# Optimization experiments

Measured on AMD Instinct MI355X. Metric: run time of the kernel, lower is better.

## Reference

```python
import jax, jax.numpy as jnp
import numpy as np

B, T, D = 2, 2048, 2048
H, KV = 16, 4
HD = D // H            # 128
REP = H // KV          # 4 query heads per kv head


def setup_inputs() -> dict:
    key = jax.random.key(0)
    ks = jax.random.split(key, 5)
    scale = D ** -0.5
    x = jax.random.normal(ks[0], (B, T, D), dtype=jnp.float32)
    Wq = jax.random.normal(ks[1], (D, H * HD), dtype=jnp.float32) * scale
    Wk = jax.random.normal(ks[2], (D, KV * HD), dtype=jnp.float32) * scale
    Wv = jax.random.normal(ks[3], (D, KV * HD), dtype=jnp.float32) * scale
    Wo = jax.random.normal(ks[4], (H * HD, D), dtype=jnp.float32) * scale
    return {"x": x, "Wq": Wq, "Wk": Wk, "Wv": Wv, "Wo": Wo}


def reference(x, Wq, Wk, Wv, Wo):
    b, t, d = x.shape
    # projections; group query heads by their kv head (repeat_interleave order:
    # q head h uses kv head h // REP, i.e. heads are contiguous per group)
    q = (x @ Wq).reshape(b, t, KV, REP, HD)          # bt(g r)d -> b t g r d
    k = (x @ Wk).reshape(b, t, KV, HD)
    v = (x @ Wv).reshape(b, t, KV, HD)
    # scores: [B, KV, REP, T, T] -- equivalent to repeat_interleave of kv heads
    scores = jnp.einsum('btgrd,bsgd->bgrts', q, k) * (HD ** -0.5)
    causal = jnp.tril(jnp.ones((t, t), dtype=bool))
    scores = jnp.where(causal, scores, -jnp.inf)
    weights = jax.nn.softmax(scores, axis=-1)
    out = jnp.einsum('bgrts,bsgd->btgrd', weights, v).reshape(b, t, H * HD)
    return jnp.round(out @ Wo, decimals=4)
```

## Files before the change

### kernel.cpp

```cpp
#include <hip/hip_runtime.h>
#include <hip/hip_bf16.h>
#include <math.h>

#define B_ 2
#define T_ 2048
#define D_ 2048
#define H_ 16
#define KV_ 4
#define HD_ 128
#define REP_ 4
#define QKVSTR 3072

typedef __attribute__((ext_vector_type(8))) short s16x8;
typedef __attribute__((ext_vector_type(4))) float f32x4;
typedef __hip_bfloat16 bf16;

__device__ __forceinline__ short f2bf(float x) {
    bf16 h = __float2bfloat16(x);
    return *reinterpret_cast<short*>(&h);
}

__device__ __forceinline__ void gl2lds16(const void* g, void* l) {
    __builtin_amdgcn_global_load_lds(
        (const __attribute__((address_space(1))) char*)g,
        (__attribute__((address_space(3))) char*)l, 16, 0, 0);
}

__global__ __launch_bounds__(256) void cast_bf16(const float* __restrict__ X,
                                                 bf16* __restrict__ Y, int n) {
    int i = (blockIdx.x * 256 + threadIdx.x) * 8;
    if (i >= n) return;
    float4 a = *(const float4*)(X + i);
    float4 b = *(const float4*)(X + i + 4);
    short o[8] = {f2bf(a.x), f2bf(a.y), f2bf(a.z), f2bf(a.w),
                  f2bf(b.x), f2bf(b.y), f2bf(b.z), f2bf(b.w)};
    *(s16x8*)(Y + i) = *(const s16x8*)o;
}

__global__ __launch_bounds__(256) void transpose_cast(const float* __restrict__ W,
                                                      bf16* __restrict__ Wt,
                                                      int K, int N, float scale) {
    __shared__ short tile[64 * 72];
    const int k0 = blockIdx.x * 64, n0 = blockIdx.y * 64;
    const int t = threadIdx.x;
    const int r = t >> 2, c0 = (t & 3) * 16;
    const float* src = W + (size_t)(k0 + r) * N + n0 + c0;
    #pragma unroll
    for (int i = 0; i < 16; i += 4) {
        float4 v = *(const float4*)(src + i);
        tile[r * 72 + c0 + i + 0] = f2bf(v.x * scale);
        tile[r * 72 + c0 + i + 1] = f2bf(v.y * scale);
        tile[r * 72 + c0 + i + 2] = f2bf(v.z * scale);
        tile[r * 72 + c0 + i + 3] = f2bf(v.w * scale);
    }
    __syncthreads();
    short tmp[16];
    #pragma unroll
    for (int i = 0; i < 16; ++i) tmp[i] = tile[(c0 + i) * 72 + r];
    bf16* dst = Wt + (size_t)(n0 + r) * K + k0 + c0;
    *(s16x8*)(dst)     = *(const s16x8*)&tmp[0];
    *(s16x8*)(dst + 8) = *(const s16x8*)&tmp[8];
}

__global__ __launch_bounds__(256) void transpose_v(const bf16* __restrict__ V,
                                                   bf16* __restrict__ Vtg) {
    __shared__ short tile[64 * 72];
    const int t0 = blockIdx.x * 64;
    const int g = blockIdx.y >> 1;
    const int dp = (blockIdx.y & 1) * 64;
    const int b = blockIdx.z;
    const int t = threadIdx.x;
    const int r = t >> 2, c0 = (t & 3) * 16;
    const bf16* src = V + (size_t)(b * T_ + t0 + r) * QKVSTR + g * HD_ + dp + c0;
    *(s16x8*)&tile[r * 72 + c0]     = *(const s16x8*)(src);
    *(s16x8*)&tile[r * 72 + c0 + 8] = *(const s16x8*)(src + 8);
    __syncthreads();
    const int d = t >> 2, tc = (t & 3) * 16;
    short tmp[16];
    #pragma unroll
    for (int i = 0; i < 16; ++i) tmp[i] = tile[(tc + i) * 72 + d];
    bf16* dst = Vtg + (size_t)((b * KV_ + g) * HD_ + dp + d) * T_ + t0 + tc;
    *(s16x8*)(dst)     = *(const s16x8*)&tmp[0];
    *(s16x8*)(dst + 8) = *(const s16x8*)&tmp[8];
}

template<typename OUTT, int ROUND>
__global__ __launch_bounds__(256) void gemm_nt(const bf16* __restrict__ A,
                                               const bf16* __restrict__ Bt,
                                               OUTT* __restrict__ C,
                                               int M, int N, int K) {
    __shared__ short As[128 * 64];
    __shared__ short Bs[128 * 64];
    const int tid = threadIdx.x;
    const int lane = tid & 63;
    const int wave = tid >> 6;
    const int quad = lane >> 4;
    const int l16 = lane & 15;
    const int wr = wave >> 1, wc = wave & 1;
    const int row0 = blockIdx.y * 128;
    const int col0 = blockIdx.x * 128;

    f32x4 acc[4][4] = {};

    for (int k0 = 0; k0 < K; k0 += 64) {
        __syncthreads();
        #pragma unroll
        for (int i = 0; i < 4; ++i) {
            int g = i * 256 + tid;
            int row = g >> 3;
            int cs = (g & 7) ^ (row & 7);
            gl2lds16(A + (size_t)(row0 + row) * K + k0 + cs * 8, &As[g * 8]);
        }
        #pragma unroll
        for (int i = 0; i < 4; ++i) {
            int g = i * 256 + tid;
            int row = g >> 3;
            int cs = (g & 7) ^ (row & 7);
            gl2lds16(Bt + (size_t)(col0 + row) * K + k0 + cs * 8, &Bs[g * 8]);
        }
        __syncthreads();
        #pragma unroll
        for (int kk = 0; kk < 2; ++kk) {
            s16x8 af[4], bfr[4];
            #pragma unroll
            for (int i = 0; i < 4; ++i) {
                int row = wr * 64 + i * 16 + l16;
                int c = (kk * 4 + quad) ^ (row & 7);
                af[i] = *(const s16x8*)&As[row * 64 + c * 8];
            }
            #pragma unroll
            for (int j = 0; j < 4; ++j) {
                int row = wc * 64 + j * 16 + l16;
                int c = (kk * 4 + quad) ^ (row & 7);
                bfr[j] = *(const s16x8*)&Bs[row * 64 + c * 8];
            }
            #pragma unroll
            for (int i = 0; i < 4; ++i)
                #pragma unroll
                for (int j = 0; j < 4; ++j)
                    acc[i][j] = __builtin_amdgcn_mfma_f32_16x16x32_bf16(
                        af[i], bfr[j], acc[i][j], 0, 0, 0);
        }
    }

    #pragma unroll
    for (int i = 0; i < 4; ++i) {
        #pragma unroll
        for (int j = 0; j < 4; ++j) {
            #pragma unroll
            for (int r = 0; r < 4; ++r) {
                int row = row0 + wr * 64 + i * 16 + quad * 4 + r;
                int col = col0 + wc * 64 + j * 16 + l16;
                float v = acc[i][j][r];
                if (ROUND) v = rintf(v * 1e4f) * 1e-4f;
                if constexpr (sizeof(OUTT) == 2)
                    C[(size_t)row * N + col] = __float2bfloat16(v);
                else
                    C[(size_t)row * N + col] = v;
            }
        }
    }
}

__global__ __launch_bounds__(256, 3) void flash3(const bf16* __restrict__ Q,
                                                 const bf16* __restrict__ K,
                                                 const bf16* __restrict__ Vtg,
                                                 bf16* __restrict__ O) {
    __shared__ short Kt[64 * 128];
    __shared__ short Vt[128 * 64];
    __shared__ short PsOb[64 * 136];
    __shared__ float lbuf[4][16];

    const int h = blockIdx.x;
    const int b = blockIdx.y & 1;
    const int qt = 31 - (blockIdx.y >> 1);
    const int g = h >> 2;
    const int tid = threadIdx.x;
    const int lane = tid & 63;
    const int wave = tid >> 6;
    const int quad = lane >> 4;
    const int l16 = lane & 15;
    const int q0g = qt * 64 + wave * 16;

    s16x8 qf[4];
    {
        const bf16* qp = Q + (size_t)(b * T_ + q0g + l16) * QKVSTR + h * HD_ + quad * 8;
        #pragma unroll
        for (int ks = 0; ks < 4; ++ks) qf[ks] = *(const s16x8*)(qp + ks * 32);
    }

    const bf16* Kp = K + (size_t)(b * T_) * QKVSTR + g * HD_;
    const bf16* Vp = Vtg + (size_t)((b * KV_ + g) * HD_) * T_;

    float l_part[4] = {0.f, 0.f, 0.f, 0.f};
    f32x4 oacc[8] = {};

    for (int j = 0; j <= qt; ++j) {
        const int s0 = j * 64;
        __syncthreads();
        #pragma unroll
        for (int i = 0; i < 4; ++i) {
            int g2 = i * 256 + tid;
            int s = g2 >> 4;
            int cs = (g2 & 15) ^ (s & 15);
            gl2lds16(Kp + (size_t)(s0 + s) * QKVSTR + cs * 8, &Kt[g2 * 8]);
        }
        #pragma unroll
        for (int i = 0; i < 4; ++i) {
            int g2 = i * 256 + tid;
            int d = g2 >> 3;
            int cs = (g2 & 7) ^ (d & 7);
            gl2lds16(Vp + (size_t)d * T_ + s0 + cs * 8, &Vt[g2 * 8]);
        }
        __syncthreads();

        f32x4 sacc[4] = {};
        #pragma unroll
        for (int ks = 0; ks < 4; ++ks) {
            s16x8 kf[4];
            #pragma unroll
            for (int ct = 0; ct < 4; ++ct) {
                int srow = ct * 16 + l16;
                int c = (ks * 4 + quad) ^ (srow & 15);
                kf[ct] = *(const s16x8*)&Kt[srow * 128 + c * 8];
            }
            #pragma unroll
            for (int ct = 0; ct < 4; ++ct)
                sacc[ct] = __builtin_amdgcn_mfma_f32_16x16x32_bf16(
                    qf[ks], kf[ct], sacc[ct], 0, 0, 0);
        }

        const bool diag = (j == qt);
        #pragma unroll
        for (int r = 0; r < 4; ++r) {
            const int qrow = q0g + quad * 4 + r;
            if (diag) {
                #pragma unroll
                for (int ct = 0; ct < 4; ++ct)
                    if (s0 + ct * 16 + l16 > qrow) sacc[ct][r] = -INFINITY;
            }
            float psum = 0.f;
            #pragma unroll
            for (int ct = 0; ct < 4; ++ct) {
                float p = exp2f(sacc[ct][r]);
                sacc[ct][r] = p;
                psum += p;
            }
            l_part[r] += psum;
        }

        #pragma unroll
        for (int ct = 0; ct < 4; ++ct)
            #pragma unroll
            for (int r = 0; r < 4; ++r)
                PsOb[(wave * 16 + quad * 4 + r) * 72 + ct * 16 + l16] = f2bf(sacc[ct][r]);

        #pragma unroll
        for (int kk = 0; kk < 2; ++kk) {
            const s16x8 pf = *(const s16x8*)&PsOb[(wave * 16 + l16) * 72 + kk * 32 + quad * 8];
            #pragma unroll
            for (int dt = 0; dt < 8; ++dt) {
                int d = dt * 16 + l16;
                int c = (kk * 4 + quad) ^ (d & 7);
                const s16x8 vf = *(const s16x8*)&Vt[d * 64 + c * 8];
                oacc[dt] = __builtin_amdgcn_mfma_f32_16x16x32_bf16(
                    vf, pf, oacc[dt], 0, 0, 0);
            }
        }
    }

    #pragma unroll
    for (int r = 0; r < 4; ++r) {
        float v = l_part[r];
        v += __shfl_xor(v, 1);
        v += __shfl_xor(v, 2);
        v += __shfl_xor(v, 4);
        v += __shfl_xor(v, 8);
        l_part[r] = v;
    }
    if (l16 == 0) {
        #pragma unroll
        for (int r = 0; r < 4; ++r) lbuf[wave][quad * 4 + r] = l_part[r];
    }
    const float invl = 1.f / lbuf[wave][l16];

    __syncthreads();

    #pragma unroll
    for (int dt = 0; dt < 8; ++dt) {
        short tmp[4];
        #pragma unroll
        for (int r = 0; r < 4; ++r) tmp[r] = f2bf(oacc[dt][r] * invl);
        *(long long*)&PsOb[(wave * 16 + l16) * 136 + dt * 16 + quad * 4] =
            *(const long long*)tmp;
    }
    const int r2 = wave * 16 + (lane >> 2);
    bf16* op = O + (size_t)(b * T_ + qt * 64 + r2) * (H_ * HD_) + h * HD_;
    #pragma unroll
    for (int c = 0; c < 4; ++c) {
        int chunk = c * 4 + (lane & 3);
        *(s16x8*)(op + chunk * 8) = *(const s16x8*)&PsOb[r2 * 136 + chunk * 8];
    }
}

extern "C" void kernel_launch(void* const* d_in, const int* in_sizes, int n_in,
                              void* d_out, int out_size, void* d_ws, size_t ws_size,
                              hipStream_t stream) {
    const float* x  = (const float*)d_in[0];
    const float* Wq = (const float*)d_in[1];
    const float* Wk = (const float*)d_in[2];
    const float* Wv = (const float*)d_in[3];
    const float* Wo = (const float*)d_in[4];
    float* out = (float*)d_out;

    const size_t NR = (size_t)B_ * T_;
    bf16* ws = (bf16*)d_ws;
    bf16* xb    = ws;
    bf16* Wqkvt = xb + NR * D_;
    bf16* Wot   = Wqkvt + (size_t)QKVSTR * D_;
    bf16* QKVb  = Wot + (size_t)D_ * D_;
    bf16* Vtg   = QKVb + NR * QKVSTR;
    bf16* Ab    = Vtg + (size_t)B_ * KV_ * HD_ * T_;

    const float qscale = 1.4426950408889634f / sqrtf((float)HD_);

    cast_bf16<<<4096, 256, 0, stream>>>(x, xb, (int)(NR * D_));
    transpose_cast<<<dim3(32, 32), 256, 0, stream>>>(Wq, Wqkvt, D_, H_ * HD_, qscale);
    transpose_cast<<<dim3(32, 8),  256, 0, stream>>>(Wk, Wqkvt + (size_t)2048 * D_, D_, KV_ * HD_, 1.f);
    transpose_cast<<<dim3(32, 8),  256, 0, stream>>>(Wv, Wqkvt + (size_t)2560 * D_, D_, KV_ * HD_, 1.f);
    transpose_cast<<<dim3(32, 32), 256, 0, stream>>>(Wo, Wot, H_ * HD_, D_, 1.f);

    gemm_nt<bf16, 0><<<dim3(QKVSTR / 128, NR / 128), 256, 0, stream>>>(
        xb, Wqkvt, QKVb, (int)NR, QKVSTR, D_);

    transpose_v<<<dim3(T_ / 64, 8, B_), 256, 0, stream>>>(QKVb + 2560, Vtg);

    flash3<<<dim3(H_, 64, 1), 256, 0, stream>>>(QKVb, QKVb + 2048, Vtg, Ab);

    gemm_nt<float, 1><<<dim3(D_ / 128, NR / 128), 256, 0, stream>>>(
        Ab, Wot, out, (int)NR, D_, H_ * HD_);
}
```

Baseline: 290.7 us.

## Merge prep kernels, shrink flash LDS for higher occupancy, reorder query tiles

The five cast and transpose launches are merged into one prep kernel that dispatches on block index, which cuts launch overhead. The flash kernel now shares one LDS buffer between K, V, P and the output staging, packs P into a swizzled 64-wide layout instead of a padded one, and replaces the LDS row-sum exchange with lane shuffles. Together these lower LDS use so four blocks per CU fit instead of three. Query tiles are scheduled in a zigzag order to balance causal work, at the cost of different ordering across the grid.

```diff
diff --git a/kernel.cpp b/kernel.cpp
--- a/kernel.cpp
+++ b/kernel.cpp
@@ -26,23 +26,33 @@
         (__attribute__((address_space(3))) char*)l, 16, 0, 0);
 }
 
-__global__ __launch_bounds__(256) void cast_bf16(const float* __restrict__ X,
-                                                 bf16* __restrict__ Y, int n) {
-    int i = (blockIdx.x * 256 + threadIdx.x) * 8;
-    if (i >= n) return;
-    float4 a = *(const float4*)(X + i);
-    float4 b = *(const float4*)(X + i + 4);
-    short o[8] = {f2bf(a.x), f2bf(a.y), f2bf(a.z), f2bf(a.w),
-                  f2bf(b.x), f2bf(b.y), f2bf(b.z), f2bf(b.w)};
-    *(s16x8*)(Y + i) = *(const s16x8*)o;
-}
-
-__global__ __launch_bounds__(256) void transpose_cast(const float* __restrict__ W,
-                                                      bf16* __restrict__ Wt,
-                                                      int K, int N, float scale) {
+__global__ __launch_bounds__(256) void prep(const float* __restrict__ x,
+                                            const float* __restrict__ Wq,
+                                            const float* __restrict__ Wk,
+                                            const float* __restrict__ Wv,
+                                            const float* __restrict__ Wo,
+                                            bf16* __restrict__ xb,
+                                            bf16* __restrict__ Wqkvt,
+                                            bf16* __restrict__ Wot,
+                                            float qscale) {
+    const int bid = blockIdx.x;
+    const int t = threadIdx.x;
+    if (bid < 4096) {
+        int i = (bid * 256 + t) * 8;
+        float4 a = *(const float4*)(x + i);
+        float4 b = *(const float4*)(x + i + 4);
+        short o[8] = {f2bf(a.x), f2bf(a.y), f2bf(a.z), f2bf(a.w),
+                      f2bf(b.x), f2bf(b.y), f2bf(b.z), f2bf(b.w)};
+        *(s16x8*)(xb + i) = *(const s16x8*)o;
+        return;
+    }
     __shared__ short tile[64 * 72];
-    const int k0 = blockIdx.x * 64, n0 = blockIdx.y * 64;
-    const int t = threadIdx.x;
+    const float* W; bf16* dst; int N; float scale; int seg;
+    if (bid < 5120)      { seg = bid - 4096; W = Wq; dst = Wqkvt;                      N = 2048; scale = qscale; }
+    else if (bid < 5376) { seg = bid - 5120; W = Wk; dst = Wqkvt + (size_t)2048 * D_;  N = 512;  scale = 1.f; }
+    else if (bid < 5632) { seg = bid - 5376; W = Wv; dst = Wqkvt + (size_t)2560 * D_;  N = 512;  scale = 1.f; }
+    else                 { seg = bid - 5632; W = Wo; dst = Wot;                        N = 2048; scale = 1.f; }
+    const int k0 = (seg & 31) * 64, n0 = (seg >> 5) * 64;
     const int r = t >> 2, c0 = (t & 3) * 16;
     const float* src = W + (size_t)(k0 + r) * N + n0 + c0;
     #pragma unroll
@@ -57,9 +67,9 @@
     short tmp[16];
     #pragma unroll
     for (int i = 0; i < 16; ++i) tmp[i] = tile[(c0 + i) * 72 + r];
-    bf16* dst = Wt + (size_t)(n0 + r) * K + k0 + c0;
-    *(s16x8*)(dst)     = *(const s16x8*)&tmp[0];
-    *(s16x8*)(dst + 8) = *(const s16x8*)&tmp[8];
+    bf16* d = dst + (size_t)(n0 + r) * D_ + k0 + c0;
+    *(s16x8*)(d)     = *(const s16x8*)&tmp[0];
+    *(s16x8*)(d + 8) = *(const s16x8*)&tmp[8];
 }
 
 __global__ __launch_bounds__(256) void transpose_v(const bf16* __restrict__ V,
@@ -162,18 +172,18 @@
     }
 }
 
-__global__ __launch_bounds__(256, 3) void flash3(const bf16* __restrict__ Q,
+__global__ __launch_bounds__(256, 4) void flash6(const bf16* __restrict__ Q,
                                                  const bf16* __restrict__ K,
                                                  const bf16* __restrict__ Vtg,
                                                  bf16* __restrict__ O) {
-    __shared__ short Kt[64 * 128];
-    __shared__ short Vt[128 * 64];
-    __shared__ short PsOb[64 * 136];
-    __shared__ float lbuf[4][16];
+    __shared__ short smem[20480];
 
     const int h = blockIdx.x;
-    const int b = blockIdx.y & 1;
-    const int qt = 31 - (blockIdx.y >> 1);
+    const int by = blockIdx.y;
+    const int b = by & 1;
+    const int u = by >> 1;
+    const int s_ = u >> 3, v_ = u & 7;
+    const int qt = (s_ >> 1) * 16 + ((s_ & 1) ? (15 - v_) : v_);
     const int g = h >> 2;
     const int tid = threadIdx.x;
     const int lane = tid & 63;
@@ -203,14 +213,14 @@
             int g2 = i * 256 + tid;
             int s = g2 >> 4;
             int cs = (g2 & 15) ^ (s & 15);
-            gl2lds16(Kp + (size_t)(s0 + s) * QKVSTR + cs * 8, &Kt[g2 * 8]);
+            gl2lds16(Kp + (size_t)(s0 + s) * QKVSTR + cs * 8, &smem[g2 * 8]);
         }
         #pragma unroll
         for (int i = 0; i < 4; ++i) {
             int g2 = i * 256 + tid;
             int d = g2 >> 3;
             int cs = (g2 & 7) ^ (d & 7);
-            gl2lds16(Vp + (size_t)d * T_ + s0 + cs * 8, &Vt[g2 * 8]);
+            gl2lds16(Vp + (size_t)d * T_ + s0 + cs * 8, &smem[8192 + g2 * 8]);
         }
         __syncthreads();
 
@@ -222,7 +232,7 @@
             for (int ct = 0; ct < 4; ++ct) {
                 int srow = ct * 16 + l16;
                 int c = (ks * 4 + quad) ^ (srow & 15);
-                kf[ct] = *(const s16x8*)&Kt[srow * 128 + c * 8];
+                kf[ct] = *(const s16x8*)&smem[srow * 128 + c * 8];
             }
             #pragma unroll
             for (int ct = 0; ct < 4; ++ct)
@@ -252,17 +262,22 @@
         #pragma unroll
         for (int ct = 0; ct < 4; ++ct)
             #pragma unroll
-            for (int r = 0; r < 4; ++r)
-                PsOb[(wave * 16 + quad * 4 + r) * 72 + ct * 16 + l16] = f2bf(sacc[ct][r]);
+            for (int r = 0; r < 4; ++r) {
+                int row = wave * 16 + quad * 4 + r;
+                int chunk = (ct * 2 + (l16 >> 3)) ^ (row & 7);
+                smem[16384 + row * 64 + chunk * 8 + (l16 & 7)] = f2bf(sacc[ct][r]);
+            }
 
         #pragma unroll
         for (int kk = 0; kk < 2; ++kk) {
-            const s16x8 pf = *(const s16x8*)&PsOb[(wave * 16 + l16) * 72 + kk * 32 + quad * 8];
+            int prow = wave * 16 + l16;
+            int pc = (kk * 4 + quad) ^ (prow & 7);
+            const s16x8 pf = *(const s16x8*)&smem[16384 + prow * 64 + pc * 8];
             #pragma unroll
             for (int dt = 0; dt < 8; ++dt) {
                 int d = dt * 16 + l16;
                 int c = (kk * 4 + quad) ^ (d & 7);
-                const s16x8 vf = *(const s16x8*)&Vt[d * 64 + c * 8];
+                const s16x8 vf = *(const s16x8*)&smem[8192 + d * 64 + c * 8];
                 oacc[dt] = __builtin_amdgcn_mfma_f32_16x16x32_bf16(
                     vf, pf, oacc[dt], 0, 0, 0);
             }
@@ -271,18 +286,21 @@
 
     #pragma unroll
     for (int r = 0; r < 4; ++r) {
-        float v = l_part[r];
-        v += __shfl_xor(v, 1);
-        v += __shfl_xor(v, 2);
-        v += __shfl_xor(v, 4);
-        v += __shfl_xor(v, 8);
-        l_part[r] = v;
-    }
-    if (l16 == 0) {
-        #pragma unroll
-        for (int r = 0; r < 4; ++r) lbuf[wave][quad * 4 + r] = l_part[r];
-    }
-    const float invl = 1.f / lbuf[wave][l16];
+        float x = l_part[r];
+        x += __shfl_xor(x, 1);
+        x += __shfl_xor(x, 2);
+        x += __shfl_xor(x, 4);
+        x += __shfl_xor(x, 8);
+        l_part[r] = x;
+    }
+    const int srcl = (l16 >> 2) << 4;
+    const float lv0 = __shfl(l_part[0], srcl);
+    const float lv1 = __shfl(l_part[1], srcl);
+    const float lv2 = __shfl(l_part[2], srcl);
+    const float lv3 = __shfl(l_part[3], srcl);
+    const int rsel = l16 & 3;
+    const float lsel = rsel == 0 ? lv0 : rsel == 1 ? lv1 : rsel == 2 ? lv2 : lv3;
+    const float invl = 1.f / lsel;
 
     __syncthreads();
 
@@ -291,7 +309,7 @@
         short tmp[4];
         #pragma unroll
         for (int r = 0; r < 4; ++r) tmp[r] = f2bf(oacc[dt][r] * invl);
-        *(long long*)&PsOb[(wave * 16 + l16) * 136 + dt * 16 + quad * 4] =
+        *(long long*)&smem[(wave * 16 + l16) * 136 + dt * 16 + quad * 4] =
             *(const long long*)tmp;
     }
     const int r2 = wave * 16 + (lane >> 2);
@@ -299,7 +317,7 @@
     #pragma unroll
     for (int c = 0; c < 4; ++c) {
         int chunk = c * 4 + (lane & 3);
-        *(s16x8*)(op + chunk * 8) = *(const s16x8*)&PsOb[r2 * 136 + chunk * 8];
+        *(s16x8*)(op + chunk * 8) = *(const s16x8*)&smem[r2 * 136 + chunk * 8];
     }
 }
 
@@ -324,18 +342,14 @@
 
     const float qscale = 1.4426950408889634f / sqrtf((float)HD_);
 
-    cast_bf16<<<4096, 256, 0, stream>>>(x, xb, (int)(NR * D_));
-    transpose_cast<<<dim3(32, 32), 256, 0, stream>>>(Wq, Wqkvt, D_, H_ * HD_, qscale);
-    transpose_cast<<<dim3(32, 8),  256, 0, stream>>>(Wk, Wqkvt + (size_t)2048 * D_, D_, KV_ * HD_, 1.f);
-    transpose_cast<<<dim3(32, 8),  256, 0, stream>>>(Wv, Wqkvt + (size_t)2560 * D_, D_, KV_ * HD_, 1.f);
-    transpose_cast<<<dim3(32, 32), 256, 0, stream>>>(Wo, Wot, H_ * HD_, D_, 1.f);
+    prep<<<6656, 256, 0, stream>>>(x, Wq, Wk, Wv, Wo, xb, Wqkvt, Wot, qscale);
 
     gemm_nt<bf16, 0><<<dim3(QKVSTR / 128, NR / 128), 256, 0, stream>>>(
         xb, Wqkvt, QKVb, (int)NR, QKVSTR, D_);
 
     transpose_v<<<dim3(T_ / 64, 8, B_), 256, 0, stream>>>(QKVb + 2560, Vtg);
 
-    flash3<<<dim3(H_, 64, 1), 256, 0, stream>>>(QKVb, QKVb + 2048, Vtg, Ab);
+    flash6<<<dim3(H_, 64), 256, 0, stream>>>(QKVb, QKVb + 2048, Vtg, Ab);
 
     gemm_nt<float, 1><<<dim3(D_ / 128, NR / 128), 256, 0, stream>>>(
         Ab, Wot, out, (int)NR, D_, H_ * HD_);
```

After: 328.1 us. 12.9% more time.
